# Optimization experiments

Measured on AMD Instinct MI355X. Metric: run time of the kernel, lower is better.

Reference implementation:

```python
import jax, jax.numpy as jnp
import numpy as np

RADIUS = 1
N_POINTS = 8


def setup_inputs() -> dict:
    key = jax.random.key(0)
    # (channels, height, width) float image in [0,1], as implied by (img*255).astype(uint8)
    x = jax.random.uniform(key, (32, 1024, 1024), dtype=jnp.float32)
    return {"x": x}


def _lbp_uniform(img, radius, n_points):
    """skimage.feature.local_binary_pattern(method='uniform') on a (C,H,W) stack.

    img holds uint8 pixel values stored as float32 (0..255).
    """
    C, H, W = img.shape
    # skimage circular sampling offsets (rounded to 5 decimals, as in skimage)
    theta = 2.0 * np.pi * np.arange(n_points) / n_points
    rp = np.round(-radius * np.sin(theta), 5)
    cp = np.round(radius * np.cos(theta), 5)

    pad = int(np.ceil(radius)) + 1  # constant-0 padding outside the image (skimage mode 'C')
    padded = jnp.pad(img, ((0, 0), (pad, pad), (pad, pad)))

    rows = jnp.arange(H, dtype=jnp.float32)
    cols = jnp.arange(W, dtype=jnp.float32)
    center = img  # (C,H,W)

    bits = []  # n_points boolean planes, each (C,H,W)
    for dr, dc in zip(rp, cp):
        r = rows + (dr + pad)  # sample row coords in padded frame, (H,)
        c = cols + (dc + pad)  # (W,)
        r0 = jnp.floor(r).astype(jnp.int32)
        c0 = jnp.floor(c).astype(jnp.int32)
        fr = (r - r0)[:, None]            # (H,1) fractional row weight
        fc = (c - c0)[None, :]            # (1,W) fractional col weight
        ri = r0[:, None]                  # (H,1) broadcast against cols
        ci = c0[None, :]                  # (1,W)
        v00 = padded[:, ri, ci]           # (C,H,W)
        v01 = padded[:, ri, ci + 1]
        v10 = padded[:, ri + 1, ci]
        v11 = padded[:, ri + 1, ci + 1]
        # bilinear interpolation of the neighbor value
        val = ((1.0 - fr) * (1.0 - fc) * v00 + (1.0 - fr) * fc * v01
               + fr * (1.0 - fc) * v10 + fr * fc * v11)
        bits.append(val - center >= 0.0)  # skimage threshold: neighbor - center >= 0

    b = jnp.stack(bits, axis=0).astype(jnp.int32)  # (P,C,H,W)
    # uniform method: count circular 0/1 transitions
    changes = jnp.sum(jnp.abs(b - jnp.roll(b, -1, axis=0)), axis=0)  # (C,H,W)
    ones = jnp.sum(b, axis=0)                                        # (C,H,W)
    lbp = jnp.where(changes <= 2, ones, n_points + 1).astype(jnp.float32)
    return lbp


def reference(x) -> jnp.ndarray:
    # (img * 255).astype(np.uint8): quantize to uint8 levels (values kept as float)
    uint8_img = jnp.clip(jnp.floor(x * 255.0), 0.0, 255.0)
    lbp_map = _lbp_uniform(uint8_img, RADIUS, N_POINTS)
    return lbp_map / 255.0
```

## Files before the change

### kernel.cpp

```cpp
#include <hip/hip_runtime.h>
#include <math.h>

#pragma clang fp contract(off)

#define OFF_A ((float)(2.0 - 0.70711))
#define OFF_B ((float)(2.0 + 0.70711))

static __device__ __forceinline__ float cvt_u8(float v) {
#pragma clang fp contract(off)
    return floorf(v * 255.0f);
}

static __device__ __forceinline__ int bilin_ge(float fr, float fc,
                                               float omr, float omc,
                                               float v00, float v01,
                                               float v10, float v11,
                                               float c) {
#pragma clang fp contract(off)
    float w00 = omr * omc;
    float w01 = omr * fc;
    float w10 = fr * omc;
    float w11 = fr * fc;
    float t0 = w00 * v00;
    float t1 = w01 * v01;
    float t2 = w10 * v10;
    float t3 = w11 * v11;
    float s1 = t0 + t1;
    float s2 = s1 + t2;
    float val = s2 + t3;
    float d = val - c;
    return d >= 0.0f;
}

__global__ __launch_bounds__(256)
void lbp_uniform_kernel4(const float* __restrict__ x, float* __restrict__ out,
                         int nquads) {
#pragma clang fp contract(off)
    int q = blockIdx.x * 256 + threadIdx.x;
    if (q >= nquads) return;

    int col0 = (q & 255) << 2;
    int row  = (q >> 8) & 1023;
    const float* img = x + ((size_t)(q >> 18) << 20);

    const float* rc = img + ((size_t)row << 10);
    bool rmv = (row > 0), rpv = (row < 1023);
    const float* rm = rmv ? rc - 1024 : rc;
    const float* rp = rpv ? rc + 1024 : rc;

    bool lv = (col0 > 0);
    bool rv = (col0 < 1020);
    int cl = lv ? col0 - 1 : col0;
    int cr = rv ? col0 + 4 : col0 + 3;

    float4 m4 = *reinterpret_cast<const float4*>(rm + col0);
    float4 c4 = *reinterpret_cast<const float4*>(rc + col0);
    float4 p4 = *reinterpret_cast<const float4*>(rp + col0);
    float mL = rm[cl], mR = rm[cr];
    float cL = rc[cl], cR = rc[cr];
    float pL = rp[cl], pR = rp[cr];

    float T[6], M[6], B[6];
    T[0] = (rmv && lv) ? cvt_u8(mL)   : 0.0f;
    T[1] = rmv         ? cvt_u8(m4.x) : 0.0f;
    T[2] = rmv         ? cvt_u8(m4.y) : 0.0f;
    T[3] = rmv         ? cvt_u8(m4.z) : 0.0f;
    T[4] = rmv         ? cvt_u8(m4.w) : 0.0f;
    T[5] = (rmv && rv) ? cvt_u8(mR)   : 0.0f;
    M[0] = lv ? cvt_u8(cL) : 0.0f;
    M[1] = cvt_u8(c4.x);
    M[2] = cvt_u8(c4.y);
    M[3] = cvt_u8(c4.z);
    M[4] = cvt_u8(c4.w);
    M[5] = rv ? cvt_u8(cR) : 0.0f;
    B[0] = (rpv && lv) ? cvt_u8(pL)   : 0.0f;
    B[1] = rpv         ? cvt_u8(p4.x) : 0.0f;
    B[2] = rpv         ? cvt_u8(p4.y) : 0.0f;
    B[3] = rpv         ? cvt_u8(p4.z) : 0.0f;
    B[4] = rpv         ? cvt_u8(p4.w) : 0.0f;
    B[5] = (rpv && rv) ? cvt_u8(pR)   : 0.0f;

    float rowf = (float)row;
    float rA = rowf + OFF_A; float frA = rA - floorf(rA);
    float rB = rowf + OFF_B; float frB = rB - floorf(rB);
    float omrA = 1.0f - frA;
    float omrB = 1.0f - frB;

    const float lut[10] = {
        (float)(0.0 / 255.0), (float)(1.0 / 255.0), (float)(2.0 / 255.0),
        (float)(3.0 / 255.0), (float)(4.0 / 255.0), (float)(5.0 / 255.0),
        (float)(6.0 / 255.0), (float)(7.0 / 255.0), (float)(8.0 / 255.0),
        (float)(9.0 / 255.0)
    };

    float res[4];
#pragma unroll
    for (int i = 0; i < 4; ++i) {
        float colf = (float)(col0 + i);
        float cA_ = colf + OFF_A; float fcA = cA_ - floorf(cA_);
        float cB_ = colf + OFF_B; float fcB = cB_ - floorf(cB_);
        float omcA = 1.0f - fcA;
        float omcB = 1.0f - fcB;

        float vNW = T[i], vN = T[i + 1], vNE = T[i + 2];
        float vW  = M[i], vC = M[i + 1], vE  = M[i + 2];
        float vSW = B[i], vS = B[i + 1], vSE = B[i + 2];

        int b0 = (vE >= vC);
        int b1 = bilin_ge(frA, fcB, omrA, omcB, vN,  vNE, vC,  vE,  vC);
        int b2 = (vN >= vC);
        int b3 = bilin_ge(frA, fcA, omrA, omcA, vNW, vN,  vW,  vC,  vC);
        int b4 = (vW >= vC);
        int b5 = bilin_ge(frB, fcA, omrB, omcA, vW,  vC,  vSW, vS,  vC);
        int b6 = (vS >= vC);
        int b7 = bilin_ge(frB, fcB, omrB, omcB, vC,  vE,  vS,  vSE, vC);

        int ones    = b0 + b1 + b2 + b3 + b4 + b5 + b6 + b7;
        int changes = (b0 ^ b1) + (b1 ^ b2) + (b2 ^ b3) + (b3 ^ b4)
                    + (b4 ^ b5) + (b5 ^ b6) + (b6 ^ b7) + (b7 ^ b0);
        int lbp = (changes <= 2) ? ones : 9;
        res[i] = lut[lbp];
    }

    float4 o;
    o.x = res[0]; o.y = res[1]; o.z = res[2]; o.w = res[3];
    *reinterpret_cast<float4*>(out + ((size_t)q << 2)) = o;
}

extern "C" void kernel_launch(void* const* d_in, const int* in_sizes, int n_in,
                              void* d_out, int out_size, void* d_ws, size_t ws_size,
                              hipStream_t stream) {
    const float* x = (const float*)d_in[0];
    float* out = (float*)d_out;
    int nquads = out_size >> 2;
    int blocks = (nquads + 255) / 256;
    lbp_uniform_kernel4<<<blocks, 256, 0, stream>>>(x, out, nquads);
}
```

Before: 262.5 us.

## Process two rows per thread and use shared-memory LBP lookup table

Each thread now computes a 4x2 output tile, so it loads 4 input rows instead of 3 per output row and reuses the column weights across both rows. The popcount/transition logic is replaced by an 8-bit pattern index into a 256-entry shared-memory table that every block builds up front. The aim is less redundant global reading and less ALU work per pixel. In exchange, each block pays for a table build and a barrier, thread count is halved, and register pressure is higher.

```diff
diff --git a/kernel.cpp b/kernel.cpp
--- a/kernel.cpp
+++ b/kernel.cpp
@@ -33,98 +33,123 @@
 }
 
 __global__ __launch_bounds__(256)
-void lbp_uniform_kernel4(const float* __restrict__ x, float* __restrict__ out,
-                         int nquads) {
+void lbp_kernel8(const float* __restrict__ x, float* __restrict__ out,
+                 int nthreads) {
 #pragma clang fp contract(off)
-    int q = blockIdx.x * 256 + threadIdx.x;
-    if (q >= nquads) return;
+    __shared__ float tbl[256];
+    {
+        int p = threadIdx.x;
+        int ones = __popc(p);
+        int rot = ((p >> 1) | (p << 7)) & 255;
+        int changes = __popc(p ^ rot);
+        int code = (changes <= 2) ? ones : 9;
+        tbl[p] = (float)code / 255.0f;
+    }
+    __syncthreads();
 
-    int col0 = (q & 255) << 2;
-    int row  = (q >> 8) & 1023;
-    const float* img = x + ((size_t)(q >> 18) << 20);
+    int idx = blockIdx.x * 256 + threadIdx.x;
+    if (idx >= nthreads) return;
 
-    const float* rc = img + ((size_t)row << 10);
-    bool rmv = (row > 0), rpv = (row < 1023);
-    const float* rm = rmv ? rc - 1024 : rc;
-    const float* rp = rpv ? rc + 1024 : rc;
+    int quad = idx & 255;
+    int rpair = (idx >> 8) & 511;
+    int ch = idx >> 17;
+    int col0 = quad << 2;
+    int row0 = rpair << 1;
 
-    bool lv = (col0 > 0);
-    bool rv = (col0 < 1020);
+    const float* img = x + ((size_t)ch << 20);
+    const float* p0 = img + ((size_t)row0 << 10);
+    const float* p1 = p0 + 1024;
+    bool gT = (row0 > 0), gB = (row0 < 1022);
+    const float* pT = gT ? p0 - 1024 : p0;
+    const float* pB = gB ? p1 + 1024 : p1;
+
+    bool lv = (col0 > 0), rv = (col0 < 1020);
     int cl = lv ? col0 - 1 : col0;
     int cr = rv ? col0 + 4 : col0 + 3;
 
-    float4 m4 = *reinterpret_cast<const float4*>(rm + col0);
-    float4 c4 = *reinterpret_cast<const float4*>(rc + col0);
-    float4 p4 = *reinterpret_cast<const float4*>(rp + col0);
-    float mL = rm[cl], mR = rm[cr];
-    float cL = rc[cl], cR = rc[cr];
-    float pL = rp[cl], pR = rp[cr];
+    float4 t4 = *reinterpret_cast<const float4*>(pT + col0);
+    float4 a4 = *reinterpret_cast<const float4*>(p0 + col0);
+    float4 b4 = *reinterpret_cast<const float4*>(p1 + col0);
+    float4 s4 = *reinterpret_cast<const float4*>(pB + col0);
+    float tL = pT[cl], tR = pT[cr];
+    float aL = p0[cl], aR = p0[cr];
+    float bL = p1[cl], bR = p1[cr];
+    float sL = pB[cl], sR = pB[cr];
 
-    float T[6], M[6], B[6];
-    T[0] = (rmv && lv) ? cvt_u8(mL)   : 0.0f;
-    T[1] = rmv         ? cvt_u8(m4.x) : 0.0f;
-    T[2] = rmv         ? cvt_u8(m4.y) : 0.0f;
-    T[3] = rmv         ? cvt_u8(m4.z) : 0.0f;
-    T[4] = rmv         ? cvt_u8(m4.w) : 0.0f;
-    T[5] = (rmv && rv) ? cvt_u8(mR)   : 0.0f;
-    M[0] = lv ? cvt_u8(cL) : 0.0f;
-    M[1] = cvt_u8(c4.x);
-    M[2] = cvt_u8(c4.y);
-    M[3] = cvt_u8(c4.z);
-    M[4] = cvt_u8(c4.w);
-    M[5] = rv ? cvt_u8(cR) : 0.0f;
-    B[0] = (rpv && lv) ? cvt_u8(pL)   : 0.0f;
-    B[1] = rpv         ? cvt_u8(p4.x) : 0.0f;
-    B[2] = rpv         ? cvt_u8(p4.y) : 0.0f;
-    B[3] = rpv         ? cvt_u8(p4.z) : 0.0f;
-    B[4] = rpv         ? cvt_u8(p4.w) : 0.0f;
-    B[5] = (rpv && rv) ? cvt_u8(pR)   : 0.0f;
+    float RT[6], R0[6], R1[6], RB[6];
+    RT[0] = (gT && lv) ? cvt_u8(tL)   : 0.0f;
+    RT[1] = gT         ? cvt_u8(t4.x) : 0.0f;
+    RT[2] = gT         ? cvt_u8(t4.y) : 0.0f;
+    RT[3] = gT         ? cvt_u8(t4.z) : 0.0f;
+    RT[4] = gT         ? cvt_u8(t4.w) : 0.0f;
+    RT[5] = (gT && rv) ? cvt_u8(tR)   : 0.0f;
+    R0[0] = lv ? cvt_u8(aL) : 0.0f;
+    R0[1] = cvt_u8(a4.x);
+    R0[2] = cvt_u8(a4.y);
+    R0[3] = cvt_u8(a4.z);
+    R0[4] = cvt_u8(a4.w);
+    R0[5] = rv ? cvt_u8(aR) : 0.0f;
+    R1[0] = lv ? cvt_u8(bL) : 0.0f;
+    R1[1] = cvt_u8(b4.x);
+    R1[2] = cvt_u8(b4.y);
+    R1[3] = cvt_u8(b4.z);
+    R1[4] = cvt_u8(b4.w);
+    R1[5] = rv ? cvt_u8(bR) : 0.0f;
+    RB[0] = (gB && lv) ? cvt_u8(sL)   : 0.0f;
+    RB[1] = gB         ? cvt_u8(s4.x) : 0.0f;
+    RB[2] = gB         ? cvt_u8(s4.y) : 0.0f;
+    RB[3] = gB         ? cvt_u8(s4.z) : 0.0f;
+    RB[4] = gB         ? cvt_u8(s4.w) : 0.0f;
+    RB[5] = (gB && rv) ? cvt_u8(sR)   : 0.0f;
 
-    float rowf = (float)row;
-    float rA = rowf + OFF_A; float frA = rA - floorf(rA);
-    float rB = rowf + OFF_B; float frB = rB - floorf(rB);
-    float omrA = 1.0f - frA;
-    float omrB = 1.0f - frB;
-
-    const float lut[10] = {
-        (float)(0.0 / 255.0), (float)(1.0 / 255.0), (float)(2.0 / 255.0),
-        (float)(3.0 / 255.0), (float)(4.0 / 255.0), (float)(5.0 / 255.0),
-        (float)(6.0 / 255.0), (float)(7.0 / 255.0), (float)(8.0 / 255.0),
-        (float)(9.0 / 255.0)
-    };
-
-    float res[4];
+    float fcA[4], fcB[4], omcA[4], omcB[4];
 #pragma unroll
     for (int i = 0; i < 4; ++i) {
         float colf = (float)(col0 + i);
-        float cA_ = colf + OFF_A; float fcA = cA_ - floorf(cA_);
-        float cB_ = colf + OFF_B; float fcB = cB_ - floorf(cB_);
-        float omcA = 1.0f - fcA;
-        float omcB = 1.0f - fcB;
-
-        float vNW = T[i], vN = T[i + 1], vNE = T[i + 2];
-        float vW  = M[i], vC = M[i + 1], vE  = M[i + 2];
-        float vSW = B[i], vS = B[i + 1], vSE = B[i + 2];
-
-        int b0 = (vE >= vC);
-        int b1 = bilin_ge(frA, fcB, omrA, omcB, vN,  vNE, vC,  vE,  vC);
-        int b2 = (vN >= vC);
-        int b3 = bilin_ge(frA, fcA, omrA, omcA, vNW, vN,  vW,  vC,  vC);
-        int b4 = (vW >= vC);
-        int b5 = bilin_ge(frB, fcA, omrB, omcA, vW,  vC,  vSW, vS,  vC);
-        int b6 = (vS >= vC);
-        int b7 = bilin_ge(frB, fcB, omrB, omcB, vC,  vE,  vS,  vSE, vC);
-
-        int ones    = b0 + b1 + b2 + b3 + b4 + b5 + b6 + b7;
-        int changes = (b0 ^ b1) + (b1 ^ b2) + (b2 ^ b3) + (b3 ^ b4)
-                    + (b4 ^ b5) + (b5 ^ b6) + (b6 ^ b7) + (b7 ^ b0);
-        int lbp = (changes <= 2) ? ones : 9;
-        res[i] = lut[lbp];
+        float cA_ = colf + OFF_A; fcA[i] = cA_ - floorf(cA_);
+        float cB_ = colf + OFF_B; fcB[i] = cB_ - floorf(cB_);
+        omcA[i] = 1.0f - fcA[i];
+        omcB[i] = 1.0f - fcB[i];
     }
 
-    float4 o;
-    o.x = res[0]; o.y = res[1]; o.z = res[2]; o.w = res[3];
-    *reinterpret_cast<float4*>(out + ((size_t)q << 2)) = o;
+    float* rows[4] = { RT, R0, R1, RB };
+    size_t obase = ((size_t)ch << 20) + ((size_t)row0 << 10) + col0;
+
+#pragma unroll
+    for (int j = 0; j < 2; ++j) {
+        float rowf = (float)(row0 + j);
+        float rA = rowf + OFF_A; float frA = rA - floorf(rA);
+        float rB_ = rowf + OFF_B; float frB = rB_ - floorf(rB_);
+        float omrA = 1.0f - frA;
+        float omrB = 1.0f - frB;
+        const float* N = rows[j];
+        const float* C = rows[j + 1];
+        const float* S = rows[j + 2];
+
+        float res[4];
+#pragma unroll
+        for (int i = 0; i < 4; ++i) {
+            float vNW = N[i], vN = N[i + 1], vNE = N[i + 2];
+            float vW  = C[i], vC = C[i + 1], vE  = C[i + 2];
+            float vSW = S[i], vS = S[i + 1], vSE = S[i + 2];
+
+            int b0 = (vE >= vC);
+            int b1 = bilin_ge(frA, fcB[i], omrA, omcB[i], vN,  vNE, vC,  vE,  vC);
+            int b2 = (vN >= vC);
+            int b3 = bilin_ge(frA, fcA[i], omrA, omcA[i], vNW, vN,  vW,  vC,  vC);
+            int b4 = (vW >= vC);
+            int b5 = bilin_ge(frB, fcA[i], omrB, omcA[i], vW,  vC,  vSW, vS,  vC);
+            int b6 = (vS >= vC);
+            int b7 = bilin_ge(frB, fcB[i], omrB, omcB[i], vC,  vE,  vS,  vSE, vC);
+
+            int pat = b0 | (b1 << 1) | (b2 << 2) | (b3 << 3)
+                    | (b4 << 4) | (b5 << 5) | (b6 << 6) | (b7 << 7);
+            res[i] = tbl[pat];
+        }
+        float4 o;
+        o.x = res[0]; o.y = res[1]; o.z = res[2]; o.w = res[3];
+        *reinterpret_cast<float4*>(out + obase + ((size_t)j << 10)) = o;
+    }
 }
 
 extern "C" void kernel_launch(void* const* d_in, const int* in_sizes, int n_in,
@@ -132,7 +157,7 @@
                               hipStream_t stream) {
     const float* x = (const float*)d_in[0];
     float* out = (float*)d_out;
-    int nquads = out_size >> 2;
-    int blocks = (nquads + 255) / 256;
-    lbp_uniform_kernel4<<<blocks, 256, 0, stream>>>(x, out, nquads);
+    int nthreads = out_size >> 3;
+    int blocks = (nthreads + 255) / 256;
+    lbp_kernel8<<<blocks, 256, 0, stream>>>(x, out, nthreads);
 }
```

Result: faster. 235.7 us (-10.2%).
